# Kernel optimization log

Hardware: AMD Instinct MI355X
Metric: run time of the kernel (lower is better)

The kernel has to match this reference:

```python
import jax, jax.numpy as jnp
import numpy as np

TOP_K = 8
N_GROUP = 8
TOPK_GROUP = 4
ROUTED_SCALING_FACTOR = 2.5
NORM_TOPK_PROB = True
TOKENS = 16384
HIDDEN = 4096
N_EXPERTS = 256


def setup_inputs() -> dict:
    key = jax.random.key(0)
    k1, k2, k3 = jax.random.split(key, 3)
    x = jax.random.normal(k1, (TOKENS, HIDDEN), dtype=jnp.float32)
    weight = jax.random.normal(k2, (N_EXPERTS, HIDDEN), dtype=jnp.float32) * 0.02
    e_score_correction_bias = jax.random.normal(k3, (N_EXPERTS,), dtype=jnp.float32) * 0.01
    return {"x": x, "weight": weight, "e_score_correction_bias": e_score_correction_bias}


def reference(x, weight, e_score_correction_bias):
    # gates: [T, E]
    gates = x @ weight.T
    orig_scores = jax.nn.sigmoid(gates.astype(jnp.float32))
    scores = orig_scores + e_score_correction_bias
    T, E = scores.shape
    eg = E // N_GROUP  # experts per group
    s = scores.reshape(T, N_GROUP, eg)
    # group score = sum of top-2 expert scores within each group -> [T, G]
    group_scores = jax.lax.top_k(s, 2)[0].sum(axis=-1)
    # torch code selects the (n_group - topk_group) SMALLEST groups and keeps
    # only those (masked_fill zeroes everything else) -- replicate faithfully.
    k_drop = N_GROUP - TOPK_GROUP
    _, bottom_idx = jax.lax.top_k(-group_scores, k_drop)  # [T, k_drop]
    keep = jnp.zeros((T, N_GROUP), dtype=bool).at[jnp.arange(T)[:, None], bottom_idx].set(True)
    s = jnp.where(keep[:, :, None], s, 0.0).reshape(T, E)
    # torch.topk(-scores) -> indices of the k SMALLEST scores
    _, inds = jax.lax.top_k(-s, TOP_K)  # [T, top_k]
    sel = jnp.take_along_axis(orig_scores, inds, axis=-1)
    if TOP_K > 1 and NORM_TOPK_PROB:
        sel = sel / (sel.sum(axis=-1, keepdims=True) + 1e-20)
    sel = sel * ROUTED_SCALING_FACTOR
    return inds, sel
```

## Files before the change

kernel.cpp:

```cpp
#include <hip/hip_runtime.h>
#include <hip/hip_fp16.h>
#include <cstdint>
#include <cmath>

#define TOKENS  16384
#define HIDDEN  4096
#define NEXP    256
#define TOPK    8
#define KDROP   4

typedef _Float16 f16x8  __attribute__((ext_vector_type(8)));
typedef _Float16 f16x4  __attribute__((ext_vector_type(4)));
typedef float    f32x16 __attribute__((ext_vector_type(16)));
typedef float    f32x4  __attribute__((ext_vector_type(4)));

#define LO_SCALE 2048.0f
#define LO_INV   (1.0f/2048.0f)

#define WS_WH_OFF 0
#define WS_WL_OFF 2097152

static __device__ __forceinline__ f32x4 ldnt4(const float* p) {
    return __builtin_nontemporal_load((const f32x4*)p);
}

__global__ __launch_bounds__(256)
void wsplit(const float* __restrict__ w, _Float16* __restrict__ wh,
            _Float16* __restrict__ wl)
{
    const int idx = blockIdx.x * 256 + threadIdx.x;
    const int e   = idx >> 9;
    const int kg8 = idx & 511;
    const float* p = w + (size_t)e * HIDDEN + kg8 * 8;
    f32x4 f0 = ldnt4(p);
    f32x4 f1 = ldnt4(p + 4);
    float v[8] = {f0.x, f0.y, f0.z, f0.w, f1.x, f1.y, f1.z, f1.w};
    f16x8 hi, lo;
    #pragma unroll
    for (int i = 0; i < 8; ++i) {
        _Float16 h = (_Float16)v[i];
        hi[i] = h;
        lo[i] = (_Float16)((v[i] - (float)h) * LO_SCALE);
    }
    const int kc = kg8 >> 2, s = (kg8 >> 1) & 1, hl = kg8 & 1;
    const int cid = ((kc * 2 + s) * 8 + (e >> 5)) * 64 + hl * 32 + (e & 31);
    ((f16x8*)wh)[cid] = hi;
    ((f16x8*)wl)[cid] = lo;
}

__device__ __forceinline__ unsigned ordkey(float f) {
    unsigned u = __float_as_uint(f);
    return (u & 0x80000000u) ? ~u : (u | 0x80000000u);
}

__global__ __launch_bounds__(256, 2)
void gemm_gate(const float* __restrict__ x, const _Float16* __restrict__ wh,
               const _Float16* __restrict__ wl,
               const float* __restrict__ bias, float* __restrict__ out)
{
    __shared__ _Float16 Ah[2][32 * 32];
    __shared__ _Float16 Al[2][32 * 32];
    __shared__ float sigbuf[32 * 256];

    const int tid  = threadIdx.x;
    const int wv   = tid >> 6;
    const int lane = tid & 63;
    const int tok0 = blockIdx.x * 32;

    const int sm = tid >> 3;
    const int sq = tid & 7;
    const float* xr = x + (size_t)(tok0 + sm) * HIDDEN + sq * 4;
    const int sidx = ((sq >> 2) * 64 + ((sq >> 1) & 1) * 32 + sm) * 8 + (sq & 1) * 4;

    const f16x8* whc = (const f16x8*)wh;
    const f16x8* wlc = (const f16x8*)wl;

    f32x16 accH[2] = {};
    f32x16 accX[2] = {};

    f16x8 bh[2][2], bl[2][2];

    {
        f32x4 a = ldnt4(xr);
        #pragma unroll
        for (int s = 0; s < 2; ++s) {
            const int base = (s * 8 + wv * 2) * 64 + lane;
            bh[s][0] = whc[base];
            bh[s][1] = whc[base + 64];
            bl[s][0] = wlc[base];
            bl[s][1] = wlc[base + 64];
        }
        f16x4 hi, lo;
        #pragma unroll
        for (int i = 0; i < 4; ++i) {
            _Float16 h = (_Float16)a[i];
            hi[i] = h;
            lo[i] = (_Float16)((a[i] - (float)h) * LO_SCALE);
        }
        *(f16x4*)&Ah[0][sidx] = hi;
        *(f16x4*)&Al[0][sidx] = lo;
    }
    __syncthreads();

    #pragma unroll 2
    for (int kc = 0; kc < 128; ++kc) {
        const int cur  = kc & 1;
        const bool more = (kc < 127);

        f32x4 an;
        f16x8 bhn[2][2], bln[2][2];
        if (more) {
            an = ldnt4(xr + (kc + 1) * 32);
            #pragma unroll
            for (int s = 0; s < 2; ++s) {
                const int base = (((kc + 1) * 2 + s) * 8 + wv * 2) * 64 + lane;
                bhn[s][0] = whc[base];
                bhn[s][1] = whc[base + 64];
                bln[s][0] = wlc[base];
                bln[s][1] = wlc[base + 64];
            }
        }

        #pragma unroll
        for (int s = 0; s < 2; ++s) {
            f16x8 ah = *(const f16x8*)&Ah[cur][(s * 64 + lane) * 8];
            f16x8 al = *(const f16x8*)&Al[cur][(s * 64 + lane) * 8];

            accH[0] = __builtin_amdgcn_mfma_f32_32x32x16_f16(ah, bh[s][0], accH[0], 0, 0, 0);
            accH[1] = __builtin_amdgcn_mfma_f32_32x32x16_f16(ah, bh[s][1], accH[1], 0, 0, 0);
            accX[0] = __builtin_amdgcn_mfma_f32_32x32x16_f16(al, bh[s][0], accX[0], 0, 0, 0);
            accX[1] = __builtin_amdgcn_mfma_f32_32x32x16_f16(al, bh[s][1], accX[1], 0, 0, 0);
            accX[0] = __builtin_amdgcn_mfma_f32_32x32x16_f16(ah, bl[s][0], accX[0], 0, 0, 0);
            accX[1] = __builtin_amdgcn_mfma_f32_32x32x16_f16(ah, bl[s][1], accX[1], 0, 0, 0);
        }

        if (more) {
            f16x4 hi, lo;
            #pragma unroll
            for (int i = 0; i < 4; ++i) {
                _Float16 h = (_Float16)an[i];
                hi[i] = h;
                lo[i] = (_Float16)((an[i] - (float)h) * LO_SCALE);
            }
            *(f16x4*)&Ah[cur ^ 1][sidx] = hi;
            *(f16x4*)&Al[cur ^ 1][sidx] = lo;
            #pragma unroll
            for (int s = 0; s < 2; ++s) {
                bh[s][0] = bhn[s][0]; bh[s][1] = bhn[s][1];
                bl[s][0] = bln[s][0]; bl[s][1] = bln[s][1];
            }
        }
        __syncthreads();
    }

    {
        const int col   = lane & 31;
        const int rbase = 4 * (lane >> 5);
        #pragma unroll
        for (int c = 0; c < 2; ++c) {
            #pragma unroll
            for (int reg = 0; reg < 16; ++reg) {
                const int row = (reg & 3) + 8 * (reg >> 2) + rbase;
                const float g = accH[c][reg] + accX[c][reg] * LO_INV;
                sigbuf[row * NEXP + wv * 64 + c * 32 + col] = 1.0f / (1.0f + expf(-g));
            }
        }
    }
    __syncthreads();

    const float4 bv = ((const float4*)bias)[lane];
    for (int tt = 0; tt < 8; ++tt) {
        const int lt = wv * 8 + tt;
        const int t  = tok0 + lt;
        f32x4 sv = *(const f32x4*)&sigbuf[lt * NEXP + lane * 4];
        const float sig0 = sv.x, sig1 = sv.y, sig2 = sv.z, sig3 = sv.w;
        const float sc0 = sig0 + bv.x, sc1 = sig1 + bv.y;
        const float sc2 = sig2 + bv.z, sc3 = sig3 + bv.w;

        float m1 = fmaxf(sc0, sc1);
        float m2 = fminf(sc0, sc1);
        if (sc2 > m1) { m2 = m1; m1 = sc2; } else m2 = fmaxf(m2, sc2);
        if (sc3 > m1) { m2 = m1; m1 = sc3; } else m2 = fmaxf(m2, sc3);
        #pragma unroll
        for (int off = 1; off < 8; off <<= 1) {
            float o1 = __shfl_xor(m1, off);
            float o2 = __shfl_xor(m2, off);
            float nm1 = fmaxf(m1, o1);
            float nm2 = fmaxf(fminf(m1, o1), fmaxf(m2, o2));
            m1 = nm1; m2 = nm2;
        }
        float gsum = m1 + m2;
        float gs[8];
        #pragma unroll
        for (int gi = 0; gi < 8; ++gi) gs[gi] = __shfl(gsum, gi * 8);

        int keepmask = 0;
        #pragma unroll
        for (int g = 0; g < 8; ++g) {
            int rank = 0;
            #pragma unroll
            for (int h = 0; h < 8; ++h)
                rank += (gs[h] < gs[g]) || (gs[h] == gs[g] && h < g);
            if (rank < KDROP) keepmask |= (1 << g);
        }
        const bool kept = (keepmask >> (lane >> 3)) & 1;

        const unsigned ib = (unsigned)(lane * 4);
        unsigned long long k0 = ((unsigned long long)ordkey(kept ? sc0 : 0.0f) << 32) | (ib + 0);
        unsigned long long k1 = ((unsigned long long)ordkey(kept ? sc1 : 0.0f) << 32) | (ib + 1);
        unsigned long long k2 = ((unsigned long long)ordkey(kept ? sc2 : 0.0f) << 32) | (ib + 2);
        unsigned long long k3 = ((unsigned long long)ordkey(kept ? sc3 : 0.0f) << 32) | (ib + 3);

        float ssum = 0.0f, myval = 0.0f;
        int myidx = 0;
        #pragma unroll
        for (int r = 0; r < TOPK; ++r) {
            unsigned long long kmin = k0 < k1 ? k0 : k1;
            if (k2 < kmin) kmin = k2;
            if (k3 < kmin) kmin = k3;
            #pragma unroll
            for (int off = 32; off >= 1; off >>= 1) {
                unsigned long long o = __shfl_xor(kmin, off);
                if (o < kmin) kmin = o;
            }
            const int id   = (int)(kmin & 0xffffffffull);
            const int src  = id >> 2;
            const int slot = id & 3;
            float vsrc = (slot == 0) ? sig0 : (slot == 1) ? sig1
                       : (slot == 2) ? sig2 : sig3;
            float v = __shfl(vsrc, src);
            ssum += v;
            if (lane == r) { myidx = id; myval = v; }
            const bool mine = (lane == src);
            if (mine && slot == 0) k0 = ~0ull;
            if (mine && slot == 1) k1 = ~0ull;
            if (mine && slot == 2) k2 = ~0ull;
            if (mine && slot == 3) k3 = ~0ull;
        }

        if (lane < TOPK) {
            out[(size_t)t * TOPK + lane] = (float)myidx;
            out[(size_t)TOKENS * TOPK + (size_t)t * TOPK + lane] =
                myval / (ssum + 1e-20f) * 2.5f;
        }
    }
}

extern "C" void kernel_launch(void* const* d_in, const int* in_sizes, int n_in,
                              void* d_out, int out_size, void* d_ws, size_t ws_size,
                              hipStream_t stream)
{
    const float* x    = (const float*)d_in[0];
    const float* w    = (const float*)d_in[1];
    const float* bias = (const float*)d_in[2];
    float* out = (float*)d_out;

    _Float16*  wh = (_Float16*)((char*)d_ws + WS_WH_OFF);
    _Float16*  wl = (_Float16*)((char*)d_ws + WS_WL_OFF);

    wsplit<<<dim3(512), dim3(256), 0, stream>>>(w, wh, wl);
    gemm_gate<<<dim3(TOKENS / 32), dim3(256), 0, stream>>>(x, wh, wl, bias, out);
}
```

Before: 489.7 us.

## Split K dimension across two wave groups per block and reduce in LDS

Doubles the block to 512 threads. Each half of the waves handles half of the hidden dimension for the same 32 tokens, and the partial gate sums are combined through shared memory before the sigmoid. The intent is more waves in flight per token tile, to hide global-load latency in the weight-streaming GEMM. In exchange it adds an extra LDS reduction pass and sync, and raises register and LDS pressure with launch bounds of 4 blocks of 512.

```diff
diff --git a/kernel.cpp b/kernel.cpp
--- a/kernel.cpp
+++ b/kernel.cpp
@@ -53,24 +53,28 @@
     return (u & 0x80000000u) ? ~u : (u | 0x80000000u);
 }
 
-__global__ __launch_bounds__(256, 2)
+__global__ __launch_bounds__(512, 4)
 void gemm_gate(const float* __restrict__ x, const _Float16* __restrict__ wh,
                const _Float16* __restrict__ wl,
                const float* __restrict__ bias, float* __restrict__ out)
 {
-    __shared__ _Float16 Ah[2][32 * 32];
-    __shared__ _Float16 Al[2][32 * 32];
+    __shared__ _Float16 Ah[2][2][32 * 32];
+    __shared__ _Float16 Al[2][2][32 * 32];
     __shared__ float sigbuf[32 * 256];
 
     const int tid  = threadIdx.x;
     const int wv   = tid >> 6;
     const int lane = tid & 63;
+    const int h    = wv >> 2;
+    const int wq   = wv & 3;
     const int tok0 = blockIdx.x * 32;
 
-    const int sm = tid >> 3;
-    const int sq = tid & 7;
-    const float* xr = x + (size_t)(tok0 + sm) * HIDDEN + sq * 4;
-    const int sidx = ((sq >> 2) * 64 + ((sq >> 1) & 1) * 32 + sm) * 8 + (sq & 1) * 4;
+    const int sm  = tid >> 3;
+    const int sq8 = tid & 7;
+    const int sh  = sq8 >> 2;
+    const int sq  = sq8 & 3;
+    const float* xr = x + (size_t)(tok0 + sm) * HIDDEN + sh * (HIDDEN / 2) + sq * 8;
+    const int schunk = (sq >> 1) * 64 + (sq & 1) * 32 + sm;
 
     const f16x8* whc = (const f16x8*)wh;
     const f16x8* wlc = (const f16x8*)wl;
@@ -80,40 +84,52 @@
 
     f16x8 bh[2][2], bl[2][2];
 
+    const bool stager = (tid < 256);
+
     {
-        f32x4 a = ldnt4(xr);
+        if (stager) {
+            f32x4 f0 = ldnt4(xr);
+            f32x4 f1 = ldnt4(xr + 4);
+            float v[8] = {f0.x, f0.y, f0.z, f0.w, f1.x, f1.y, f1.z, f1.w};
+            f16x8 hi, lo;
+            #pragma unroll
+            for (int i = 0; i < 8; ++i) {
+                _Float16 hh = (_Float16)v[i];
+                hi[i] = hh;
+                lo[i] = (_Float16)((v[i] - (float)hh) * LO_SCALE);
+            }
+            *(f16x8*)&Ah[sh][0][schunk * 8] = hi;
+            *(f16x8*)&Al[sh][0][schunk * 8] = lo;
+        }
+        const int kc = h * 64;
         #pragma unroll
         for (int s = 0; s < 2; ++s) {
-            const int base = (s * 8 + wv * 2) * 64 + lane;
+            const int base = ((kc * 2 + s) * 8 + wq * 2) * 64 + lane;
             bh[s][0] = whc[base];
             bh[s][1] = whc[base + 64];
             bl[s][0] = wlc[base];
             bl[s][1] = wlc[base + 64];
         }
-        f16x4 hi, lo;
-        #pragma unroll
-        for (int i = 0; i < 4; ++i) {
-            _Float16 h = (_Float16)a[i];
-            hi[i] = h;
-            lo[i] = (_Float16)((a[i] - (float)h) * LO_SCALE);
-        }
-        *(f16x4*)&Ah[0][sidx] = hi;
-        *(f16x4*)&Al[0][sidx] = lo;
     }
     __syncthreads();
 
     #pragma unroll 2
-    for (int kc = 0; kc < 128; ++kc) {
-        const int cur  = kc & 1;
-        const bool more = (kc < 127);
-
-        f32x4 an;
+    for (int i = 0; i < 64; ++i) {
+        const int cur  = i & 1;
+        const bool more = (i < 63);
+
+        f32x4 a0n, a1n;
         f16x8 bhn[2][2], bln[2][2];
         if (more) {
-            an = ldnt4(xr + (kc + 1) * 32);
+            if (stager) {
+                const float* ap = xr + (i + 1) * 32;
+                a0n = ldnt4(ap);
+                a1n = ldnt4(ap + 4);
+            }
+            const int kc = h * 64 + i + 1;
             #pragma unroll
             for (int s = 0; s < 2; ++s) {
-                const int base = (((kc + 1) * 2 + s) * 8 + wv * 2) * 64 + lane;
+                const int base = ((kc * 2 + s) * 8 + wq * 2) * 64 + lane;
                 bhn[s][0] = whc[base];
                 bhn[s][1] = whc[base + 64];
                 bln[s][0] = wlc[base];
@@ -123,8 +139,8 @@
 
         #pragma unroll
         for (int s = 0; s < 2; ++s) {
-            f16x8 ah = *(const f16x8*)&Ah[cur][(s * 64 + lane) * 8];
-            f16x8 al = *(const f16x8*)&Al[cur][(s * 64 + lane) * 8];
+            f16x8 ah = *(const f16x8*)&Ah[h][cur][(s * 64 + lane) * 8];
+            f16x8 al = *(const f16x8*)&Al[h][cur][(s * 64 + lane) * 8];
 
             accH[0] = __builtin_amdgcn_mfma_f32_32x32x16_f16(ah, bh[s][0], accH[0], 0, 0, 0);
             accH[1] = __builtin_amdgcn_mfma_f32_32x32x16_f16(ah, bh[s][1], accH[1], 0, 0, 0);
@@ -135,15 +151,18 @@
         }
 
         if (more) {
-            f16x4 hi, lo;
-            #pragma unroll
-            for (int i = 0; i < 4; ++i) {
-                _Float16 h = (_Float16)an[i];
-                hi[i] = h;
-                lo[i] = (_Float16)((an[i] - (float)h) * LO_SCALE);
-            }
-            *(f16x4*)&Ah[cur ^ 1][sidx] = hi;
-            *(f16x4*)&Al[cur ^ 1][sidx] = lo;
+            if (stager) {
+                float v[8] = {a0n.x, a0n.y, a0n.z, a0n.w, a1n.x, a1n.y, a1n.z, a1n.w};
+                f16x8 hi, lo;
+                #pragma unroll
+                for (int ii = 0; ii < 8; ++ii) {
+                    _Float16 hh = (_Float16)v[ii];
+                    hi[ii] = hh;
+                    lo[ii] = (_Float16)((v[ii] - (float)hh) * LO_SCALE);
+                }
+                *(f16x8*)&Ah[sh][cur ^ 1][schunk * 8] = hi;
+                *(f16x8*)&Al[sh][cur ^ 1][schunk * 8] = lo;
+            }
             #pragma unroll
             for (int s = 0; s < 2; ++s) {
                 bh[s][0] = bhn[s][0]; bh[s][1] = bhn[s][1];
@@ -154,23 +173,35 @@
     }
 
     {
-        const int col   = lane & 31;
+        const int col   = wq * 64 + (lane & 31);
         const int rbase = 4 * (lane >> 5);
-        #pragma unroll
-        for (int c = 0; c < 2; ++c) {
-            #pragma unroll
-            for (int reg = 0; reg < 16; ++reg) {
-                const int row = (reg & 3) + 8 * (reg >> 2) + rbase;
-                const float g = accH[c][reg] + accX[c][reg] * LO_INV;
-                sigbuf[row * NEXP + wv * 64 + c * 32 + col] = 1.0f / (1.0f + expf(-g));
-            }
-        }
-    }
-    __syncthreads();
+        if (h == 0) {
+            #pragma unroll
+            for (int c = 0; c < 2; ++c)
+                #pragma unroll
+                for (int reg = 0; reg < 16; ++reg) {
+                    const int row = (reg & 3) + 8 * (reg >> 2) + rbase;
+                    sigbuf[row * NEXP + col + c * 32] = accH[c][reg] + accX[c][reg] * LO_INV;
+                }
+        }
+        __syncthreads();
+        if (h == 1) {
+            #pragma unroll
+            for (int c = 0; c < 2; ++c)
+                #pragma unroll
+                for (int reg = 0; reg < 16; ++reg) {
+                    const int row = (reg & 3) + 8 * (reg >> 2) + rbase;
+                    const float g = sigbuf[row * NEXP + col + c * 32]
+                                  + accH[c][reg] + accX[c][reg] * LO_INV;
+                    sigbuf[row * NEXP + col + c * 32] = 1.0f / (1.0f + expf(-g));
+                }
+        }
+        __syncthreads();
+    }
 
     const float4 bv = ((const float4*)bias)[lane];
-    for (int tt = 0; tt < 8; ++tt) {
-        const int lt = wv * 8 + tt;
+    for (int tt = 0; tt < 4; ++tt) {
+        const int lt = wv * 4 + tt;
         const int t  = tok0 + lt;
         f32x4 sv = *(const f32x4*)&sigbuf[lt * NEXP + lane * 4];
         const float sig0 = sv.x, sig1 = sv.y, sig2 = sv.z, sig3 = sv.w;
@@ -199,8 +230,8 @@
         for (int g = 0; g < 8; ++g) {
             int rank = 0;
             #pragma unroll
-            for (int h = 0; h < 8; ++h)
-                rank += (gs[h] < gs[g]) || (gs[h] == gs[g] && h < g);
+            for (int hh = 0; hh < 8; ++hh)
+                rank += (gs[hh] < gs[g]) || (gs[hh] == gs[g] && hh < g);
             if (rank < KDROP) keepmask |= (1 << g);
         }
         const bool kept = (keepmask >> (lane >> 3)) & 1;
@@ -259,5 +290,5 @@
     _Float16*  wl = (_Float16*)((char*)d_ws + WS_WL_OFF);
 
     wsplit<<<dim3(512), dim3(256), 0, stream>>>(w, wh, wl);
-    gemm_gate<<<dim3(TOKENS / 32), dim3(256), 0, stream>>>(x, wh, wl, bias, out);
-}
+    gemm_gate<<<dim3(TOKENS / 32), dim3(512), 0, stream>>>(x, wh, wl, bias, out);
+}
```

Result: slower. 793.9 us (+62.1%).
